# Optimization experiments

Hardware: AMD Instinct MI355X
Metric: run time of the kernel (lower is better)

The kernel has to match this reference:

```python
import jax, jax.numpy as jnp
import numpy as np

N_NODES = 100000
IMPROVED_FILL = 2.0  # PyG improved=True self-loop weight


def setup_inputs() -> dict:
    key = jax.random.key(0)
    k1, k2, k3, k4 = jax.random.split(key, 4)
    x = jax.random.normal(k1, (N_NODES, 128), dtype=jnp.float32)
    edge_index = jax.random.randint(k2, (2, 1600000), 0, N_NODES, dtype=jnp.int64)
    edge_weight = jax.random.uniform(k3, (1600000,), dtype=jnp.float32)
    W = jax.random.normal(k4, (128, 64), dtype=jnp.float32) * (1.0 / np.sqrt(128.0))
    b = jnp.zeros((64,), dtype=jnp.float32)
    return {"x": x, "edge_index": edge_index, "edge_weight": edge_weight, "W": W, "b": b}


def reference(x, edge_index, edge_weight, W, b):
    N = x.shape[0]
    row, col = edge_index[0], edge_index[1]
    # add self-loops with fill value 2.0 (improved=True)
    loop = jnp.arange(N, dtype=edge_index.dtype)
    row_f = jnp.concatenate([row, loop])
    col_f = jnp.concatenate([col, loop])
    ew_f = jnp.concatenate([edge_weight, jnp.full((N,), IMPROVED_FILL, dtype=x.dtype)])
    # symmetric degree normalization (degree computed at target/col, per PyG gcn_norm)
    deg = jax.ops.segment_sum(ew_f, col_f, num_segments=N)  # [N]
    dinv = jnp.where(deg > 0, jax.lax.rsqrt(deg), 0.0)
    norm = dinv[row_f] * ew_f * dinv[col_f]  # [E+N]
    # linear transform first, then gather-scale-scatter aggregation, then bias
    xw = x @ W  # [N, 64]
    msgs = xw[row_f] * norm[:, None]  # [E+N, 64]
    out = jax.ops.segment_sum(msgs, col_f, num_segments=N) + b  # [N, 64]
    # act is None -> returns (x, embedding), both equal to out
    return (out, out)
```

## Files before the change

### kernel.cpp

```cpp
#include <hip/hip_runtime.h>

#define F_IN 128
#define F_OUT 64

#define NBK_SHIFT 7
#define NB_MAX    800
#define CAP       2432
#define CHUNK     3200

__device__ __forceinline__ unsigned short f2bf(float f) {
    unsigned u = __float_as_uint(f);
    u += 0x7FFFu + ((u >> 16) & 1u);
    return (unsigned short)(u >> 16);
}
__device__ __forceinline__ float bf2f(unsigned short h) {
    return __uint_as_float((unsigned)h << 16);
}

__global__ __launch_bounds__(256) void part_kernel(const int* __restrict__ rowi,
                                                   const int* __restrict__ coli,
                                                   const float* __restrict__ ew,
                                                   int* __restrict__ gcursor,
                                                   unsigned int* __restrict__ regA,
                                                   unsigned char* __restrict__ regB,
                                                   int E, int NB) {
    __shared__ unsigned long long rec[CHUNK];
    __shared__ int off0[NB_MAX];
    __shared__ int cur[NB_MAX];
    __shared__ int gbase[NB_MAX];
    __shared__ int ps[256];

    const int t = threadIdx.x;
    const int start = blockIdx.x * CHUNK;
    int cntE = E - start;
    if (cntE > CHUNK) cntE = CHUNK;
    if (cntE < 0) cntE = 0;

    for (int i = t; i < NB; i += 256) cur[i] = 0;
    __syncthreads();

    #pragma unroll 4
    for (int i = t; i < cntE; i += 256)
        atomicAdd(&cur[coli[start + i] >> NBK_SHIFT], 1);
    __syncthreads();

    int v0 = 0, v1 = 0, v2 = 0, v3 = 0, tsum;
    {
        int b0 = t << 2;
        if (b0 + 0 < NB) v0 = cur[b0 + 0];
        if (b0 + 1 < NB) v1 = cur[b0 + 1];
        if (b0 + 2 < NB) v2 = cur[b0 + 2];
        if (b0 + 3 < NB) v3 = cur[b0 + 3];
    }
    tsum = v0 + v1 + v2 + v3;
    ps[t] = tsum;
    __syncthreads();
    for (int off = 1; off < 256; off <<= 1) {
        int a = (t >= off) ? ps[t - off] : 0;
        __syncthreads();
        ps[t] += a;
        __syncthreads();
    }
    {
        int e0 = ps[t] - tsum;
        int b0 = t << 2;
        if (b0 + 0 < NB) off0[b0 + 0] = e0;            e0 += v0;
        if (b0 + 1 < NB) off0[b0 + 1] = e0;            e0 += v1;
        if (b0 + 2 < NB) off0[b0 + 2] = e0;            e0 += v2;
        if (b0 + 3 < NB) off0[b0 + 3] = e0;
    }
    __syncthreads();

    for (int i = t; i < NB; i += 256) {
        int c = cur[i];
        gbase[i] = (c > 0) ? atomicAdd(&gcursor[i], c) : 0;
        cur[i] = off0[i];
    }
    __syncthreads();

    #pragma unroll 2
    for (int i = t; i < cntE; i += 256) {
        int c = coli[start + i];
        int r = rowi[start + i];
        float w = ew[start + i];
        unsigned q = (unsigned)(w * 32767.0f + 0.5f);
        int b = c >> NBK_SHIFT;
        int p = atomicAdd(&cur[b], 1);
        rec[p] = ((unsigned long long)(unsigned)c << 32) |
                 (((unsigned)r << 15) | q);
    }
    __syncthreads();

    #pragma unroll 2
    for (int i = t; i < cntE; i += 256) {
        unsigned long long rv = rec[i];
        int c = (int)(rv >> 32);
        int b = c >> NBK_SHIFT;
        int gp = gbase[b] + (i - off0[b]);
        if (gp < CAP) {
            size_t idx = (size_t)b * CAP + gp;
            regA[idx] = (unsigned)rv;
            regB[idx] = (unsigned char)(c & 127);
        }
    }
}

__global__ __launch_bounds__(256) void bucket_kernel(const int* __restrict__ gcursor,
                                                     const unsigned int* __restrict__ regA,
                                                     const unsigned char* __restrict__ regB,
                                                     unsigned int* __restrict__ recC,
                                                     unsigned int* __restrict__ info,
                                                     float* __restrict__ dinv, int N) {
    __shared__ unsigned long long pk[128];
    __shared__ int sc[128];
    __shared__ int cur[128];
    __shared__ unsigned int lrec[CAP];

    const int b = blockIdx.x;
    const int t = threadIdx.x;
    if (t < 128) pk[t] = 0ULL;
    __syncthreads();

    int nE = gcursor[b];
    if (nE > CAP) nE = CAP;
    const size_t basee = (size_t)b * CAP;

    unsigned va[10];
    unsigned vc[10];
    #pragma unroll
    for (int j = 0; j < 10; ++j) {
        const int i = t + (j << 8);
        if (i < nE) {
            unsigned a  = regA[basee + i];
            unsigned lc = regB[basee + i];
            va[j] = a; vc[j] = lc;
            atomicAdd(&pk[lc], (1ULL << 42) |
                               ((unsigned long long)(a & 32767u) << 15));
        }
    }
    __syncthreads();

    if (t < 128) sc[t] = (int)(pk[t] >> 42);
    __syncthreads();
    for (int off = 1; off < 128; off <<= 1) {
        int vv = 0;
        if (t < 128 && t >= off) vv = sc[t - off];
        __syncthreads();
        if (t < 128) sc[t] += vv;
        __syncthreads();
    }
    if (t < 128) cur[t] = sc[t] - (int)(pk[t] >> 42);
    __syncthreads();

    #pragma unroll
    for (int j = 0; j < 10; ++j) {
        const int i = t + (j << 8);
        if (i < nE) {
            int p = atomicAdd(&cur[vc[j]], 1);
            lrec[p] = va[j];
        }
    }
    __syncthreads();

    for (int i = t; i < nE; i += 256) recC[basee + i] = lrec[i];

    if (t < 128) {
        const int c = (b << NBK_SHIFT) + t;
        if (c < N) {
            unsigned long long pv = pk[t];
            float sw = (float)((double)(pv & ((1ULL << 42) - 1)) * (1.0 / 1073741824.0));
            dinv[c] = rsqrtf(2.0f + sw);
            int cc = (int)(pv >> 42);
            int ls = sc[t] - cc;
            if (cc > 64) cc = 64;
            info[c] = ((unsigned)ls << 7) | (unsigned)cc;
        }
    }
}

#define XS_STRIDE 132
#define FMA4(acc, sc, wv)                      \
    acc.x = fmaf(sc, wv.x, acc.x);             \
    acc.y = fmaf(sc, wv.y, acc.y);             \
    acc.z = fmaf(sc, wv.z, acc.z);             \
    acc.w = fmaf(sc, wv.w, acc.w);

__global__ __launch_bounds__(256) void gemm_kernel(const float* __restrict__ x,
                                                   const float* __restrict__ W,
                                                   const float* __restrict__ dinv,
                                                   unsigned short* __restrict__ ybf, int N) {
    __shared__ float xs[64 * XS_STRIDE];

    const int tid = threadIdx.x;
    const int rx  = tid & 15;
    const int cx  = tid >> 4;
    const int base = blockIdx.x * 64;

    const float4* xg = (const float4*)x;
    for (int i = tid; i < 64 * (F_IN / 4); i += 256) {
        int r  = i >> 5;
        int k4 = i & 31;
        if (base + r < N)
            *(float4*)&xs[r * XS_STRIDE + (k4 << 2)] = xg[((size_t)(base + r) << 5) + k4];
    }
    __syncthreads();

    float4 acc0 = {0,0,0,0}, acc1 = {0,0,0,0}, acc2 = {0,0,0,0}, acc3 = {0,0,0,0};

    const float* xp = &xs[rx * XS_STRIDE];
    const float4* Wg4 = (const float4*)W;
    const int cb = cx;

    #pragma unroll 2
    for (int k4 = 0; k4 < 32; ++k4) {
        const int k0 = k4 << 2;
        float4 a0 = *(const float4*)(xp + 0 * 16 * XS_STRIDE + k0);
        float4 a1 = *(const float4*)(xp + 1 * 16 * XS_STRIDE + k0);
        float4 a2 = *(const float4*)(xp + 2 * 16 * XS_STRIDE + k0);
        float4 a3 = *(const float4*)(xp + 3 * 16 * XS_STRIDE + k0);
        float4 b0 = Wg4[(size_t)(k0 + 0) * 16 + cb];
        float4 b1 = Wg4[(size_t)(k0 + 1) * 16 + cb];
        float4 b2 = Wg4[(size_t)(k0 + 2) * 16 + cb];
        float4 b3 = Wg4[(size_t)(k0 + 3) * 16 + cb];
        FMA4(acc0, a0.x, b0) FMA4(acc0, a0.y, b1) FMA4(acc0, a0.z, b2) FMA4(acc0, a0.w, b3)
        FMA4(acc1, a1.x, b0) FMA4(acc1, a1.y, b1) FMA4(acc1, a1.z, b2) FMA4(acc1, a1.w, b3)
        FMA4(acc2, a2.x, b0) FMA4(acc2, a2.y, b1) FMA4(acc2, a2.z, b2) FMA4(acc2, a2.w, b3)
        FMA4(acc3, a3.x, b0) FMA4(acc3, a3.y, b1) FMA4(acc3, a3.z, b2) FMA4(acc3, a3.w, b3)
    }

    #pragma unroll
    for (int j = 0; j < 4; ++j) {
        const int r = base + rx + 16 * j;
        if (r < N) {
            float d = dinv[r];
            float4 a = (j == 0) ? acc0 : (j == 1) ? acc1 : (j == 2) ? acc2 : acc3;
            ushort4 o;
            o.x = f2bf(a.x * d);
            o.y = f2bf(a.y * d);
            o.z = f2bf(a.z * d);
            o.w = f2bf(a.w * d);
            *(ushort4*)&ybf[((size_t)r << 6) + (cb << 2)] = o;
        }
    }
}

__global__ __launch_bounds__(256) void aggregate_kernel(const unsigned int* __restrict__ info,
                                                        const unsigned int* __restrict__ recC,
                                                        const unsigned short* __restrict__ ybf,
                                                        const float* __restrict__ dinv,
                                                        const float* __restrict__ b,
                                                        float* __restrict__ out, int N) {
    const int lane = threadIdx.x & 63;
    const int v = blockIdx.x * 4 + (threadIdx.x >> 6);
    if (v >= N) return;

    const int es = lane >> 4;
    const int fl = lane & 15;

    const unsigned inf = info[v];
    int n = inf & 127;
    if (n > 64) n = 64;
    const size_t rbase = (size_t)(v >> NBK_SHIFT) * CAP + (inf >> 7);

    const float dv = dinv[v];
    const ushort4 yv = *(const ushort4*)&ybf[((size_t)v << 6) + (fl << 2)];
    const float4 bb = *(const float4*)&b[fl << 2];

    unsigned mv = 0;
    if (lane < n) mv = recC[rbase + lane];

    float4 acc = {0, 0, 0, 0};
    for (int i = 0; i < n; i += 16) {
        unsigned m0 = (unsigned)__shfl((int)mv, i + es);
        unsigned m1 = (unsigned)__shfl((int)mv, i + 4 + es);
        unsigned m2 = (unsigned)__shfl((int)mv, i + 8 + es);
        unsigned m3 = (unsigned)__shfl((int)mv, i + 12 + es);
        bool k0 = (i + es) < n;
        bool k1 = (i + 4 + es) < n;
        bool k2 = (i + 8 + es) < n;
        bool k3 = (i + 12 + es) < n;
        ushort4 a0 = {0,0,0,0}, a1 = {0,0,0,0}, a2 = {0,0,0,0}, a3 = {0,0,0,0};
        if (k0) a0 = *(const ushort4*)&ybf[((size_t)(m0 >> 15) << 6) + (fl << 2)];
        if (k1) a1 = *(const ushort4*)&ybf[((size_t)(m1 >> 15) << 6) + (fl << 2)];
        if (k2) a2 = *(const ushort4*)&ybf[((size_t)(m2 >> 15) << 6) + (fl << 2)];
        if (k3) a3 = *(const ushort4*)&ybf[((size_t)(m3 >> 15) << 6) + (fl << 2)];
        if (k0) {
            float w0 = (float)(m0 & 32767u) * (1.f / 32767.f);
            acc.x = fmaf(w0, bf2f(a0.x), acc.x);
            acc.y = fmaf(w0, bf2f(a0.y), acc.y);
            acc.z = fmaf(w0, bf2f(a0.z), acc.z);
            acc.w = fmaf(w0, bf2f(a0.w), acc.w);
        }
        if (k1) {
            float w1 = (float)(m1 & 32767u) * (1.f / 32767.f);
            acc.x = fmaf(w1, bf2f(a1.x), acc.x);
            acc.y = fmaf(w1, bf2f(a1.y), acc.y);
            acc.z = fmaf(w1, bf2f(a1.z), acc.z);
            acc.w = fmaf(w1, bf2f(a1.w), acc.w);
        }
        if (k2) {
            float w2 = (float)(m2 & 32767u) * (1.f / 32767.f);
            acc.x = fmaf(w2, bf2f(a2.x), acc.x);
            acc.y = fmaf(w2, bf2f(a2.y), acc.y);
            acc.z = fmaf(w2, bf2f(a2.z), acc.z);
            acc.w = fmaf(w2, bf2f(a2.w), acc.w);
        }
        if (k3) {
            float w3 = (float)(m3 & 32767u) * (1.f / 32767.f);
            acc.x = fmaf(w3, bf2f(a3.x), acc.x);
            acc.y = fmaf(w3, bf2f(a3.y), acc.y);
            acc.z = fmaf(w3, bf2f(a3.z), acc.z);
            acc.w = fmaf(w3, bf2f(a3.w), acc.w);
        }
    }

    acc.x += __shfl_xor(acc.x, 16); acc.y += __shfl_xor(acc.y, 16);
    acc.z += __shfl_xor(acc.z, 16); acc.w += __shfl_xor(acc.w, 16);
    acc.x += __shfl_xor(acc.x, 32); acc.y += __shfl_xor(acc.y, 32);
    acc.z += __shfl_xor(acc.z, 32); acc.w += __shfl_xor(acc.w, 32);

    if (lane < 16) {
        float4 val;
        val.x = fmaf(dv, 2.f * bf2f(yv.x) + acc.x, bb.x);
        val.y = fmaf(dv, 2.f * bf2f(yv.y) + acc.y, bb.y);
        val.z = fmaf(dv, 2.f * bf2f(yv.z) + acc.z, bb.z);
        val.w = fmaf(dv, 2.f * bf2f(yv.w) + acc.w, bb.w);
        *(float4*)&out[((size_t)v << 6) + (fl << 2)]       = val;
        *(float4*)&out[((size_t)(N + v) << 6) + (fl << 2)] = val;
    }
}

extern "C" void kernel_launch(void* const* d_in, const int* in_sizes, int n_in,
                              void* d_out, int out_size, void* d_ws, size_t ws_size,
                              hipStream_t stream) {
    const float* x  = (const float*)d_in[0];
    const int*   ei = (const int*)d_in[1];
    const float* ew = (const float*)d_in[2];
    const float* W  = (const float*)d_in[3];
    const float* b  = (const float*)d_in[4];

    const int N = in_sizes[0] / F_IN;
    const int E = in_sizes[2];

    const int* rowi = ei;
    const int* coli = ei + E;
    float* out = (float*)d_out;

    const int NB = (N + 127) >> NBK_SHIFT;
    if (NB > NB_MAX) return;

    const int Npad = (N + 255) & ~255;
    char* p = (char*)d_ws;
    unsigned short* ybf  = (unsigned short*)p;  p += (size_t)N * F_OUT * 2;
    unsigned int*   regA = (unsigned int*)p;    p += (size_t)NB * CAP * 4;
    unsigned int*   recC = (unsigned int*)p;    p += (size_t)NB * CAP * 4;
    unsigned int*   info = (unsigned int*)p;    p += (size_t)Npad * 4;
    float* dinv = (float*)p;                    p += (size_t)Npad * 4;
    int*   gcur = (int*)p;                      p += (size_t)NB_MAX * 4;
    unsigned char* regB = (unsigned char*)p;

    hipMemsetAsync(gcur, 0, (size_t)NB * sizeof(int), stream);

    const int P = (E + CHUNK - 1) / CHUNK;
    part_kernel<<<P, 256, 0, stream>>>(rowi, coli, ew, gcur, regA, regB, E, NB);
    bucket_kernel<<<NB, 256, 0, stream>>>(gcur, regA, regB, recC, info, dinv, N);

    gemm_kernel<<<(N + 63) / 64, 256, 0, stream>>>(x, W, dinv, ybf, N);

    aggregate_kernel<<<(N + 3) / 4, 256, 0, stream>>>(info, recC, ybf, dinv, b, out, N);
}
```

Baseline: 228.5 us.

## Use split-bf16 MFMA for the GEMM and per-lane feature aggregation

The fp32 FMA GEMM becomes MFMA 16x16x32 bf16 instructions with a hi/lo split (three MFMAs per tile) to keep near-fp32 accuracy. W is converted into hi/lo bf16 tiles in shared memory and outputs are staged through LDS for coalesced 16-byte stores. The aggregation kernel is also restructured so each lane owns one output feature and processes 8 neighbours per iteration with 2-byte loads, removing the cross-lane reductions. This trades wider vector loads for narrower per-lane gathers, and removes the clamp of n to 64.

```diff
diff --git a/kernel.cpp b/kernel.cpp
--- a/kernel.cpp
+++ b/kernel.cpp
@@ -16,6 +16,9 @@
 __device__ __forceinline__ float bf2f(unsigned short h) {
     return __uint_as_float((unsigned)h << 16);
 }
+
+typedef __attribute__((ext_vector_type(8))) short bf16x8;
+typedef __attribute__((ext_vector_type(4))) float f32x4;
 
 __global__ __launch_bounds__(256) void part_kernel(const int* __restrict__ rowi,
                                                    const int* __restrict__ coli,
@@ -178,68 +181,93 @@
     }
 }
 
-#define XS_STRIDE 132
-#define FMA4(acc, sc, wv)                      \
-    acc.x = fmaf(sc, wv.x, acc.x);             \
-    acc.y = fmaf(sc, wv.y, acc.y);             \
-    acc.z = fmaf(sc, wv.z, acc.z);             \
-    acc.w = fmaf(sc, wv.w, acc.w);
+#define KP 136
+#define OP 72
 
 __global__ __launch_bounds__(256) void gemm_kernel(const float* __restrict__ x,
                                                    const float* __restrict__ W,
                                                    const float* __restrict__ dinv,
                                                    unsigned short* __restrict__ ybf, int N) {
-    __shared__ float xs[64 * XS_STRIDE];
-
-    const int tid = threadIdx.x;
-    const int rx  = tid & 15;
-    const int cx  = tid >> 4;
+    __shared__ unsigned short smem[2 * 64 * KP];
+    unsigned short* Wh = smem;
+    unsigned short* Wl = smem + 64 * KP;
+
+    const int tid  = threadIdx.x;
+    const int lane = tid & 63;
+    const int w    = tid >> 6;
     const int base = blockIdx.x * 64;
 
-    const float4* xg = (const float4*)x;
-    for (int i = tid; i < 64 * (F_IN / 4); i += 256) {
-        int r  = i >> 5;
-        int k4 = i & 31;
-        if (base + r < N)
-            *(float4*)&xs[r * XS_STRIDE + (k4 << 2)] = xg[((size_t)(base + r) << 5) + k4];
-    }
-    __syncthreads();
-
-    float4 acc0 = {0,0,0,0}, acc1 = {0,0,0,0}, acc2 = {0,0,0,0}, acc3 = {0,0,0,0};
-
-    const float* xp = &xs[rx * XS_STRIDE];
-    const float4* Wg4 = (const float4*)W;
-    const int cb = cx;
-
-    #pragma unroll 2
-    for (int k4 = 0; k4 < 32; ++k4) {
-        const int k0 = k4 << 2;
-        float4 a0 = *(const float4*)(xp + 0 * 16 * XS_STRIDE + k0);
-        float4 a1 = *(const float4*)(xp + 1 * 16 * XS_STRIDE + k0);
-        float4 a2 = *(const float4*)(xp + 2 * 16 * XS_STRIDE + k0);
-        float4 a3 = *(const float4*)(xp + 3 * 16 * XS_STRIDE + k0);
-        float4 b0 = Wg4[(size_t)(k0 + 0) * 16 + cb];
-        float4 b1 = Wg4[(size_t)(k0 + 1) * 16 + cb];
-        float4 b2 = Wg4[(size_t)(k0 + 2) * 16 + cb];
-        float4 b3 = Wg4[(size_t)(k0 + 3) * 16 + cb];
-        FMA4(acc0, a0.x, b0) FMA4(acc0, a0.y, b1) FMA4(acc0, a0.z, b2) FMA4(acc0, a0.w, b3)
-        FMA4(acc1, a1.x, b0) FMA4(acc1, a1.y, b1) FMA4(acc1, a1.z, b2) FMA4(acc1, a1.w, b3)
-        FMA4(acc2, a2.x, b0) FMA4(acc2, a2.y, b1) FMA4(acc2, a2.z, b2) FMA4(acc2, a2.w, b3)
-        FMA4(acc3, a3.x, b0) FMA4(acc3, a3.y, b1) FMA4(acc3, a3.z, b2) FMA4(acc3, a3.w, b3)
-    }
-
-    #pragma unroll
-    for (int j = 0; j < 4; ++j) {
-        const int r = base + rx + 16 * j;
-        if (r < N) {
-            float d = dinv[r];
-            float4 a = (j == 0) ? acc0 : (j == 1) ? acc1 : (j == 2) ? acc2 : acc3;
-            ushort4 o;
-            o.x = f2bf(a.x * d);
-            o.y = f2bf(a.y * d);
-            o.z = f2bf(a.z * d);
-            o.w = f2bf(a.w * d);
-            *(ushort4*)&ybf[((size_t)r << 6) + (cb << 2)] = o;
+    for (int i = tid; i < F_IN * F_OUT; i += 256) {
+        int k = i >> 6, c = i & 63;
+        float f = W[i];
+        unsigned short h = f2bf(f);
+        Wh[c * KP + k] = h;
+        Wl[c * KP + k] = f2bf(f - bf2f(h));
+    }
+    __syncthreads();
+
+    const int rg = lane & 15;
+    const int g  = lane >> 4;
+
+    int row = base + 16 * w + rg;
+    if (row > N - 1) row = N - 1;
+    const float* xrow = x + (size_t)row * F_IN;
+
+    f32x4 acc0 = {0.f, 0.f, 0.f, 0.f};
+    f32x4 acc1 = acc0, acc2 = acc0, acc3 = acc0;
+
+    #pragma unroll
+    for (int ks = 0; ks < 4; ++ks) {
+        const int k8 = ks * 32 + g * 8;
+        float4 xa = *(const float4*)(xrow + k8);
+        float4 xb = *(const float4*)(xrow + k8 + 4);
+        float fs[8] = {xa.x, xa.y, xa.z, xa.w, xb.x, xb.y, xb.z, xb.w};
+        bf16x8 ah, al;
+        #pragma unroll
+        for (int j = 0; j < 8; ++j) {
+            unsigned short h = f2bf(fs[j]);
+            ah[j] = (short)h;
+            al[j] = (short)f2bf(fs[j] - bf2f(h));
+        }
+        #define DO_TILE(T, ACC) {                                              \
+            const int cb_ = ((T) * 16 + rg) * KP + k8;                         \
+            bf16x8 bh_ = *(const bf16x8*)&Wh[cb_];                             \
+            bf16x8 bl_ = *(const bf16x8*)&Wl[cb_];                             \
+            ACC = __builtin_amdgcn_mfma_f32_16x16x32_bf16(ah, bh_, ACC, 0,0,0);\
+            ACC = __builtin_amdgcn_mfma_f32_16x16x32_bf16(al, bh_, ACC, 0,0,0);\
+            ACC = __builtin_amdgcn_mfma_f32_16x16x32_bf16(ah, bl_, ACC, 0,0,0);\
+        }
+        DO_TILE(0, acc0) DO_TILE(1, acc1) DO_TILE(2, acc2) DO_TILE(3, acc3)
+        #undef DO_TILE
+    }
+
+    float dv[4];
+    #pragma unroll
+    for (int i = 0; i < 4; ++i) {
+        int rr = base + 16 * w + 4 * g + i;
+        dv[i] = dinv[(rr < N) ? rr : (N - 1)];
+    }
+
+    __syncthreads();
+    unsigned short* outl = smem;
+
+    #define ST_TILE(T, ACC) {                                                  \
+        _Pragma("unroll")                                                      \
+        for (int i = 0; i < 4; ++i)                                            \
+            outl[(16 * w + 4 * g + i) * OP + (T) * 16 + rg] =                  \
+                f2bf(ACC[i] * dv[i]);                                          \
+    }
+    ST_TILE(0, acc0) ST_TILE(1, acc1) ST_TILE(2, acc2) ST_TILE(3, acc3)
+    #undef ST_TILE
+    __syncthreads();
+
+    #pragma unroll
+    for (int rep = 0; rep < 2; ++rep) {
+        int cid = tid + (rep << 8);
+        int r = cid >> 3, s = cid & 7;
+        if (base + r < N) {
+            uint4 val = *(const uint4*)&outl[r * OP + s * 8];
+            *(uint4*)&ybf[((size_t)(base + r) << 6) + (s << 3)] = val;
         }
     }
 }
@@ -254,80 +282,40 @@
     const int v = blockIdx.x * 4 + (threadIdx.x >> 6);
     if (v >= N) return;
 
-    const int es = lane >> 4;
-    const int fl = lane & 15;
-
     const unsigned inf = info[v];
-    int n = inf & 127;
-    if (n > 64) n = 64;
+    const int n = inf & 127;
     const size_t rbase = (size_t)(v >> NBK_SHIFT) * CAP + (inf >> 7);
 
-    const float dv = dinv[v];
-    const ushort4 yv = *(const ushort4*)&ybf[((size_t)v << 6) + (fl << 2)];
-    const float4 bb = *(const float4*)&b[fl << 2];
-
-    unsigned mv = 0;
-    if (lane < n) mv = recC[rbase + lane];
-
-    float4 acc = {0, 0, 0, 0};
-    for (int i = 0; i < n; i += 16) {
-        unsigned m0 = (unsigned)__shfl((int)mv, i + es);
-        unsigned m1 = (unsigned)__shfl((int)mv, i + 4 + es);
-        unsigned m2 = (unsigned)__shfl((int)mv, i + 8 + es);
-        unsigned m3 = (unsigned)__shfl((int)mv, i + 12 + es);
-        bool k0 = (i + es) < n;
-        bool k1 = (i + 4 + es) < n;
-        bool k2 = (i + 8 + es) < n;
-        bool k3 = (i + 12 + es) < n;
-        ushort4 a0 = {0,0,0,0}, a1 = {0,0,0,0}, a2 = {0,0,0,0}, a3 = {0,0,0,0};
-        if (k0) a0 = *(const ushort4*)&ybf[((size_t)(m0 >> 15) << 6) + (fl << 2)];
-        if (k1) a1 = *(const ushort4*)&ybf[((size_t)(m1 >> 15) << 6) + (fl << 2)];
-        if (k2) a2 = *(const ushort4*)&ybf[((size_t)(m2 >> 15) << 6) + (fl << 2)];
-        if (k3) a3 = *(const ushort4*)&ybf[((size_t)(m3 >> 15) << 6) + (fl << 2)];
-        if (k0) {
-            float w0 = (float)(m0 & 32767u) * (1.f / 32767.f);
-            acc.x = fmaf(w0, bf2f(a0.x), acc.x);
-            acc.y = fmaf(w0, bf2f(a0.y), acc.y);
-            acc.z = fmaf(w0, bf2f(a0.z), acc.z);
-            acc.w = fmaf(w0, bf2f(a0.w), acc.w);
-        }
-        if (k1) {
-            float w1 = (float)(m1 & 32767u) * (1.f / 32767.f);
-            acc.x = fmaf(w1, bf2f(a1.x), acc.x);
-            acc.y = fmaf(w1, bf2f(a1.y), acc.y);
-            acc.z = fmaf(w1, bf2f(a1.z), acc.z);
-            acc.w = fmaf(w1, bf2f(a1.w), acc.w);
-        }
-        if (k2) {
-            float w2 = (float)(m2 & 32767u) * (1.f / 32767.f);
-            acc.x = fmaf(w2, bf2f(a2.x), acc.x);
-            acc.y = fmaf(w2, bf2f(a2.y), acc.y);
-            acc.z = fmaf(w2, bf2f(a2.z), acc.z);
-            acc.w = fmaf(w2, bf2f(a2.w), acc.w);
-        }
-        if (k3) {
-            float w3 = (float)(m3 & 32767u) * (1.f / 32767.f);
-            acc.x = fmaf(w3, bf2f(a3.x), acc.x);
-            acc.y = fmaf(w3, bf2f(a3.y), acc.y);
-            acc.z = fmaf(w3, bf2f(a3.z), acc.z);
-            acc.w = fmaf(w3, bf2f(a3.w), acc.w);
-        }
-    }
-
-    acc.x += __shfl_xor(acc.x, 16); acc.y += __shfl_xor(acc.y, 16);
-    acc.z += __shfl_xor(acc.z, 16); acc.w += __shfl_xor(acc.w, 16);
-    acc.x += __shfl_xor(acc.x, 32); acc.y += __shfl_xor(acc.y, 32);
-    acc.z += __shfl_xor(acc.z, 32); acc.w += __shfl_xor(acc.w, 32);
-
-    if (lane < 16) {
-        float4 val;
-        val.x = fmaf(dv, 2.f * bf2f(yv.x) + acc.x, bb.x);
-        val.y = fmaf(dv, 2.f * bf2f(yv.y) + acc.y, bb.y);
-        val.z = fmaf(dv, 2.f * bf2f(yv.z) + acc.z, bb.z);
-        val.w = fmaf(dv, 2.f * bf2f(yv.w) + acc.w, bb.w);
-        *(float4*)&out[((size_t)v << 6) + (fl << 2)]       = val;
-        *(float4*)&out[((size_t)(N + v) << 6) + (fl << 2)] = val;
-    }
+    const float dv  = dinv[v];
+    const float bl  = b[lane];
+    const float yvl = bf2f(ybf[((size_t)v << 6) + lane]);
+
+    int mv = 0;
+    if (lane < n) mv = (int)recC[rbase + lane];
+
+    float acc = 0.f;
+    for (int i = 0; i < n; i += 8) {
+        int mm[8];
+        #pragma unroll
+        for (int j = 0; j < 8; ++j) mm[j] = __shfl(mv, i + j);
+        unsigned short aa[8];
+        #pragma unroll
+        for (int j = 0; j < 8; ++j)
+            aa[j] = (i + j < n)
+                  ? ybf[((size_t)((unsigned)mm[j] >> 15) << 6) + lane]
+                  : (unsigned short)0;
+        #pragma unroll
+        for (int j = 0; j < 8; ++j) {
+            if (i + j < n) {
+                float ww = (float)(mm[j] & 32767) * (1.f / 32767.f);
+                acc = fmaf(ww, bf2f(aa[j]), acc);
+            }
+        }
+    }
+
+    const float val = fmaf(dv, 2.f * yvl + acc, bl);
+    out[((size_t)v << 6) + lane]       = val;
+    out[((size_t)(N + v) << 6) + lane] = val;
 }
 
 extern "C" void kernel_launch(void* const* d_in, const int* in_sizes, int n_in,
```

New measurement: 253.3 us. 10.9% more time.
